# Kernel optimization log

Measured on AMD Instinct MI355X. Metric: run time of the kernel, lower is better.

The kernel has to match this reference:

```python
import jax, jax.numpy as jnp
import numpy as np

N = 50000          # nodes
E = 800000         # edges (avg degree 16)
F = 128            # in_dim = num_hidden*heads = pred_dim
H = 4              # attention heads per layer
D = 32             # num_hidden (per-head dim)
R = 11             # rel_num
L = 2              # num_layers
SCALE = float(1.0 / np.sqrt(D))


def setup_inputs() -> dict:
    key = jax.random.key(0)
    ks = jax.random.split(key, 16)
    inputs = jax.random.normal(ks[0], (N, F), jnp.float32)
    edge_types = jax.random.randint(ks[1], (E,), 0, R)
    src = jax.random.randint(ks[2], (E,), 0, N)
    dst = jax.random.randint(ks[3], (E,), 0, N)
    centrality = jax.random.uniform(ks[4], (N,), jnp.float32)
    rel_emb = jax.random.normal(ks[5], (R, F), jnp.float32) * 0.1
    # stacked per-layer projection weights (both layers have F -> H*D = F)
    Wq = jax.random.normal(ks[6], (L, F, H * D), jnp.float32) * 0.05
    Wk = jax.random.normal(ks[7], (L, F, H * D), jnp.float32) * 0.05
    Wv = jax.random.normal(ks[8], (L, F, H * D), jnp.float32) * 0.05
    We = jax.random.normal(ks[9], (L, F, H * D), jnp.float32) * 0.05
    bq = jnp.zeros((L, H * D), jnp.float32)
    bk = jnp.zeros((L, H * D), jnp.float32)
    bv = jnp.zeros((L, H * D), jnp.float32)
    be = jnp.zeros((L, H * D), jnp.float32)
    W_out = jax.random.normal(ks[10], (H * D, 1), jnp.float32) * 0.05
    b_out = jnp.zeros((1,), jnp.float32)
    gamma = jnp.ones((1,), jnp.float32)
    beta = jnp.zeros((1,), jnp.float32)
    return {"inputs": inputs, "edge_types": edge_types, "src": src, "dst": dst,
            "centrality": centrality, "rel_emb": rel_emb,
            "Wq": Wq, "bq": bq, "Wk": Wk, "bk": bk, "Wv": Wv, "bv": bv,
            "We": We, "be": be, "W_out": W_out, "b_out": b_out,
            "gamma": gamma, "beta": beta}


def _segment_softmax(score, dst, n):
    # score: [E, H]; softmax over incoming edges of each dst node
    m = jax.ops.segment_max(score, dst, num_segments=n)          # [N, H]
    ex = jnp.exp(score - m[dst])                                  # [E, H]
    s = jax.ops.segment_sum(ex, dst, num_segments=n)              # [N, H]
    return ex / (s[dst] + 1e-9)


def reference(inputs, edge_types, src, dst, centrality, rel_emb,
              Wq, bq, Wk, bk, Wv, bv, We, be, W_out, b_out, gamma, beta):
    h = inputs                                   # [N, F]
    ef = rel_emb[edge_types]                     # [E, pred_dim] relational edge embedding
    for l in range(L):
        q = (h @ Wq[l] + bq[l]).reshape(N, H, D)
        k = (h @ Wk[l] + bk[l]).reshape(N, H, D)
        v = (h @ Wv[l] + bv[l]).reshape(N, H, D)
        e = (ef @ We[l] + be[l]).reshape(E, H, D)
        # edge_mode="add": edge features added to keys/values on each edge
        ke = k[src] + e                           # [E, H, D]
        score = jnp.sum(q[dst] * ke, axis=-1) * SCALE   # [E, H]
        attn = _segment_softmax(score, dst, N)          # [E, H]
        msg = attn[:, :, None] * (v[src] + e)           # [E, H, D]
        agg = jax.ops.segment_sum(msg, dst, num_segments=N)  # [N, H, D]
        # identity residual (in_dim == H*D) + ELU activation
        h = jax.nn.elu(agg.reshape(N, H * D) + h)
    logits = h @ W_out + b_out                    # [N, 1]
    logits = jax.nn.relu((centrality * gamma + beta)[:, None] * logits)
    return logits
```

## Files before the change

### kernel.cpp

```cpp
#include <hip/hip_runtime.h>
#include <hip/hip_bf16.h>
#include <math.h>

#define SCALE_C 0.17677669529663687f
#define CAPP 64

typedef short bf16x8 __attribute__((ext_vector_type(8)));
typedef float f32x4 __attribute__((ext_vector_type(4)));


__global__ __launch_bounds__(256) void prep_scatter_k(
    const float* __restrict__ Wq, const float* __restrict__ Wk, const float* __restrict__ Wv,
    __hip_bfloat16* __restrict__ wf,
    const float* __restrict__ rel_emb, const float* __restrict__ We, const float* __restrict__ be,
    float* __restrict__ re, int R, int reb,
    const int* __restrict__ dst, const int* __restrict__ src, const int* __restrict__ etype,
    int E, int* __restrict__ cnt, int* __restrict__ bins) {
  int b = blockIdx.x;
  if (b < 48) {
    int tid = b * 256 + threadIdx.x;
    int lane = tid & 63;
    int frag = tid >> 6;
    int ks = frag & 3;
    int ct = (frag >> 2) & 7;
    int mat = frag >> 5;
    int l = mat / 3, m = mat % 3;
    const float* W = ((m == 0) ? Wq : (m == 1) ? Wk : Wv) + (size_t)l * 128 * 128;
    int nn = ct * 16 + (lane & 15);
    int k0 = ks * 32 + (lane >> 4) * 8;
    __hip_bfloat16 tmp[8];
    #pragma unroll
    for (int j = 0; j < 8; ++j) tmp[j] = __float2bfloat16(W[(size_t)(k0 + j) * 128 + nn]);
    *(uint4*)&wf[(size_t)frag * 64 * 8 + (size_t)lane * 8] = *(const uint4*)tmp;
  } else if (b < 48 + reb) {
    int idx = (b - 48) * 256 + threadIdx.x;
    int tot = 2 * R * 128;
    if (idx >= tot) return;
    int c = idx & 127;
    int r = (idx >> 7) % R;
    int l = idx / (R * 128);
    const float* W = We + (size_t)l * 128 * 128;
    float acc = be[l * 128 + c];
    #pragma unroll 4
    for (int kk = 0; kk < 128; ++kk) acc += rel_emb[r * 128 + kk] * W[kk * 128 + c];
    re[idx] = acc;
  } else {
    int e = (b - 48 - reb) * 256 + threadIdx.x;
    if (e < E) {
      int d = dst[e];
      int pos = atomicAdd(&cnt[d], 1);
      if (pos < CAPP) bins[(d << 6) + pos] = src[e] | (etype[e] << 20);
    }
  }
}


__device__ __forceinline__ void qkv_body(
    const float* __restrict__ Xf, const __hip_bfloat16* __restrict__ Xb,
    const __hip_bfloat16* __restrict__ wf,
    const float* __restrict__ bq, const float* __restrict__ bk, const float* __restrict__ bv,
    __hip_bfloat16* __restrict__ qo, __hip_bfloat16* __restrict__ kvo, int n, int bid) {
  __shared__ __hip_bfloat16 kvt[2][32][264];
  int wid = threadIdx.x >> 6;
  int lane = threadIdx.x & 63;
  int row0 = bid * 64 + wid * 32;
  if (row0 >= n) return;
  int cl = lane & 15;
  int quad = lane >> 4;

  bf16x8 afrag[2][4];
  #pragma unroll
  for (int s = 0; s < 2; ++s) {
    int arow = row0 + s * 16 + cl;
    bool av = arow < n;
    if (Xb) {
      const __hip_bfloat16* xr = Xb + (size_t)arow * 128 + quad * 8;
      #pragma unroll
      for (int ks = 0; ks < 4; ++ks) {
        uint4 raw = av ? *(const uint4*)(xr + ks * 32) : make_uint4(0, 0, 0, 0);
        afrag[s][ks] = __builtin_bit_cast(bf16x8, raw);
      }
    } else {
      const float* xr = Xf + (size_t)arow * 128 + quad * 8;
      #pragma unroll
      for (int ks = 0; ks < 4; ++ks) {
        float4 x0 = av ? *(const float4*)(xr + ks * 32)     : make_float4(0.f, 0.f, 0.f, 0.f);
        float4 x1 = av ? *(const float4*)(xr + ks * 32 + 4) : make_float4(0.f, 0.f, 0.f, 0.f);
        union { bf16x8 v; __hip_bfloat16 h[8]; } fu;
        fu.h[0] = __float2bfloat16(x0.x); fu.h[1] = __float2bfloat16(x0.y);
        fu.h[2] = __float2bfloat16(x0.z); fu.h[3] = __float2bfloat16(x0.w);
        fu.h[4] = __float2bfloat16(x1.x); fu.h[5] = __float2bfloat16(x1.y);
        fu.h[6] = __float2bfloat16(x1.z); fu.h[7] = __float2bfloat16(x1.w);
        afrag[s][ks] = fu.v;
      }
    }
  }
  const uint4* wfu = (const uint4*)wf;

  #pragma unroll
  for (int ct = 0; ct < 8; ++ct) {
    f32x4 a0 = {0.f, 0.f, 0.f, 0.f}, a1 = {0.f, 0.f, 0.f, 0.f};
    #pragma unroll
    for (int ks = 0; ks < 4; ++ks) {
      uint4 braw = wfu[((size_t)ct * 4 + ks) * 64 + lane];
      bf16x8 bfr = __builtin_bit_cast(bf16x8, braw);
      a0 = __builtin_amdgcn_mfma_f32_16x16x32_bf16(afrag[0][ks], bfr, a0, 0, 0, 0);
      a1 = __builtin_amdgcn_mfma_f32_16x16x32_bf16(afrag[1][ks], bfr, a1, 0, 0, 0);
    }
    int c = ct * 16 + cl;
    float bb = bq[c];
    #pragma unroll
    for (int r = 0; r < 4; ++r) {
      kvt[wid][quad * 4 + r][c]      = __float2bfloat16((a0[r] + bb) * SCALE_C);
      kvt[wid][16 + quad * 4 + r][c] = __float2bfloat16((a1[r] + bb) * SCALE_C);
    }
  }
  {
    const uint4* tsrc = (const uint4*)&kvt[wid][0][0];
    #pragma unroll
    for (int it = 0; it < 8; ++it) {
      int idx = it * 64 + lane;
      int row = idx >> 4, g = idx & 15;
      if (row0 + row < n)
        *(uint4*)&qo[((size_t)(row0 + row)) * 128 + g * 8] = tsrc[row * 33 + g];
    }
  }

  #pragma unroll
  for (int m = 1; m <= 2; ++m) {
    const float* bias = (m == 1) ? bk : bv;
    #pragma unroll
    for (int ct = 0; ct < 8; ++ct) {
      f32x4 a0 = {0.f, 0.f, 0.f, 0.f}, a1 = {0.f, 0.f, 0.f, 0.f};
      #pragma unroll
      for (int ks = 0; ks < 4; ++ks) {
        uint4 braw = wfu[((size_t)(m * 8 + ct) * 4 + ks) * 64 + lane];
        bf16x8 bfr = __builtin_bit_cast(bf16x8, braw);
        a0 = __builtin_amdgcn_mfma_f32_16x16x32_bf16(afrag[0][ks], bfr, a0, 0, 0, 0);
        a1 = __builtin_amdgcn_mfma_f32_16x16x32_bf16(afrag[1][ks], bfr, a1, 0, 0, 0);
      }
      int c = ct * 16 + cl;
      float bb = bias[c];
      int p = 8 * (c >> 2) + (c & 3) + ((m == 2) ? 4 : 0);
      #pragma unroll
      for (int r = 0; r < 4; ++r) {
        kvt[wid][quad * 4 + r][p]      = __float2bfloat16(a0[r] + bb);
        kvt[wid][16 + quad * 4 + r][p] = __float2bfloat16(a1[r] + bb);
      }
    }
  }
  {
    const uint4* tsrc = (const uint4*)&kvt[wid][0][0];
    #pragma unroll
    for (int it = 0; it < 16; ++it) {
      int idx = it * 64 + lane;
      int row = idx >> 5, off = idx & 31;
      if (row0 + row < n)
        *(uint4*)&kvo[((size_t)(row0 + row)) * 256 + off * 8] = tsrc[row * 33 + off];
    }
  }
}

__global__ __launch_bounds__(128) void qkv1_k(
    const float* __restrict__ Xf, const __hip_bfloat16* __restrict__ wf,
    const float* __restrict__ bq, const float* __restrict__ bk, const float* __restrict__ bv,
    __hip_bfloat16* __restrict__ qo, __hip_bfloat16* __restrict__ kvo, int n) {
  qkv_body(Xf, nullptr, wf, bq, bk, bv, qo, kvo, n, blockIdx.x);
}

__global__ __launch_bounds__(128) void qkv2_k(
    const __hip_bfloat16* __restrict__ Xb, const __hip_bfloat16* __restrict__ wf,
    const float* __restrict__ bq, const float* __restrict__ bk, const float* __restrict__ bv,
    __hip_bfloat16* __restrict__ qo, __hip_bfloat16* __restrict__ kvo, int n) {
  qkv_body(nullptr, Xb, wf, bq, bk, bv, qo, kvo, n, blockIdx.x);
}


__global__ __launch_bounds__(256) void edge_k(
    const __hip_bfloat16* __restrict__ qb, const __hip_bfloat16* __restrict__ kv,
    const float* __restrict__ re,
    const int* __restrict__ bins, const int* __restrict__ cnt,
    const float* __restrict__ h_in_f, const __hip_bfloat16* __restrict__ h_in_b,
    __hip_bfloat16* __restrict__ h_out_b,
    const float* __restrict__ Wout, const float* __restrict__ bout,
    const float* __restrict__ cent, const float* __restrict__ gamma,
    const float* __restrict__ beta, float* __restrict__ outp, int n) {
  int node = blockIdx.x * 4 + (threadIdx.x >> 6);
  if (node >= n) return;
  int lane = threadIdx.x & 63;
  int j = lane & 15;
  int quarter = lane >> 4;
  int rs = node << 6;
  int deg = cnt[node];
  deg = deg < CAPP ? deg : CAPP;

  uint4 qraw = *((const uint4*)(qb + ((size_t)node << 7)) + j);
  float qa0 = __uint_as_float(qraw.x << 16), qa1 = __uint_as_float(qraw.x & 0xffff0000u);
  float qa2 = __uint_as_float(qraw.y << 16), qa3 = __uint_as_float(qraw.y & 0xffff0000u);
  float qa4 = __uint_as_float(qraw.z << 16), qa5 = __uint_as_float(qraw.z & 0xffff0000u);
  float qa6 = __uint_as_float(qraw.w << 16), qa7 = __uint_as_float(qraw.w & 0xffff0000u);

  float ssum = 0.f;
  float acc0 = 0.f, acc1 = 0.f, acc2 = 0.f, acc3 = 0.f;
  float acc4 = 0.f, acc5 = 0.f, acc6 = 0.f, acc7 = 0.f;
  int nit = (deg + 3) >> 2;

  int pk1 = (quarter < deg) ? bins[rs + quarter] : 0;
  int pk2 = (quarter + 4 < deg) ? bins[rs + quarter + 4] : 0;
  uint s0 = (uint)pk1 & 0xFFFFFu, t0 = (uint)pk1 >> 20;
  const uint4* kr0 = (const uint4*)kv + (s0 * 32u + (uint)(j * 2));
  uint4 raw0 = kr0[0];
  uint4 raw1 = kr0[1];
  const float4* rr0 = (const float4*)re + (t0 * 32u + (uint)(j * 2));
  float4 r0 = rr0[0];
  float4 r1 = rr0[1];
  pk1 = pk2;

  for (int i = 0; i < nit; ++i) {
    int e2 = 4 * (i + 2) + quarter;
    pk2 = (e2 < deg) ? bins[rs + e2] : 0;
    uint s1 = (uint)pk1 & 0xFFFFFu, t1 = (uint)pk1 >> 20;
    const uint4* krn = (const uint4*)kv + (s1 * 32u + (uint)(j * 2));
    uint4 nraw0 = krn[0];
    uint4 nraw1 = krn[1];
    const float4* rrn = (const float4*)re + (t1 * 32u + (uint)(j * 2));
    float4 nr0 = rrn[0];
    float4 nr1 = rrn[1];

    bool valid = 4 * i + quarter < deg;
    float k0 = __uint_as_float(raw0.x << 16);
    float k1 = __uint_as_float(raw0.x & 0xffff0000u);
    float k2 = __uint_as_float(raw0.y << 16);
    float k3 = __uint_as_float(raw0.y & 0xffff0000u);
    float v0 = __uint_as_float(raw0.z << 16);
    float v1 = __uint_as_float(raw0.z & 0xffff0000u);
    float v2 = __uint_as_float(raw0.w << 16);
    float v3 = __uint_as_float(raw0.w & 0xffff0000u);
    float k4 = __uint_as_float(raw1.x << 16);
    float k5 = __uint_as_float(raw1.x & 0xffff0000u);
    float k6 = __uint_as_float(raw1.y << 16);
    float k7 = __uint_as_float(raw1.y & 0xffff0000u);
    float v4 = __uint_as_float(raw1.z << 16);
    float v5 = __uint_as_float(raw1.z & 0xffff0000u);
    float v6 = __uint_as_float(raw1.w << 16);
    float v7 = __uint_as_float(raw1.w & 0xffff0000u);
    float p = qa0 * (k0 + r0.x) + qa1 * (k1 + r0.y) + qa2 * (k2 + r0.z) + qa3 * (k3 + r0.w)
            + qa4 * (k4 + r1.x) + qa5 * (k5 + r1.y) + qa6 * (k6 + r1.z) + qa7 * (k7 + r1.w);
    p += __shfl_xor(p, 1);
    p += __shfl_xor(p, 2);
    float w = valid ? __expf(p) : 0.f;
    ssum += w;
    acc0 += w * (v0 + r0.x);
    acc1 += w * (v1 + r0.y);
    acc2 += w * (v2 + r0.z);
    acc3 += w * (v3 + r0.w);
    acc4 += w * (v4 + r1.x);
    acc5 += w * (v5 + r1.y);
    acc6 += w * (v6 + r1.z);
    acc7 += w * (v7 + r1.w);

    raw0 = nraw0; raw1 = nraw1; r0 = nr0; r1 = nr1;
    pk1 = pk2;
  }
  ssum += __shfl_xor(ssum, 16); ssum += __shfl_xor(ssum, 32);
  acc0 += __shfl_xor(acc0, 16); acc0 += __shfl_xor(acc0, 32);
  acc1 += __shfl_xor(acc1, 16); acc1 += __shfl_xor(acc1, 32);
  acc2 += __shfl_xor(acc2, 16); acc2 += __shfl_xor(acc2, 32);
  acc3 += __shfl_xor(acc3, 16); acc3 += __shfl_xor(acc3, 32);
  acc4 += __shfl_xor(acc4, 16); acc4 += __shfl_xor(acc4, 32);
  acc5 += __shfl_xor(acc5, 16); acc5 += __shfl_xor(acc5, 32);
  acc6 += __shfl_xor(acc6, 16); acc6 += __shfl_xor(acc6, 32);
  acc7 += __shfl_xor(acc7, 16); acc7 += __shfl_xor(acc7, 32);
  if (quarter != 0) return;

  float inv = 1.f / (ssum + 1e-9f);
  float4 h0, h1;
  if (h_in_b) {
    uint4 hraw = *((const uint4*)(h_in_b + ((size_t)node << 7)) + j);
    h0.x = __uint_as_float(hraw.x << 16); h0.y = __uint_as_float(hraw.x & 0xffff0000u);
    h0.z = __uint_as_float(hraw.y << 16); h0.w = __uint_as_float(hraw.y & 0xffff0000u);
    h1.x = __uint_as_float(hraw.z << 16); h1.y = __uint_as_float(hraw.z & 0xffff0000u);
    h1.z = __uint_as_float(hraw.w << 16); h1.w = __uint_as_float(hraw.w & 0xffff0000u);
  } else {
    const float4* hrow = (const float4*)h_in_f + ((uint)node * 32u + (uint)(j * 2));
    h0 = hrow[0]; h1 = hrow[1];
  }
  float x0 = acc0 * inv + h0.x;
  float x1 = acc1 * inv + h0.y;
  float x2 = acc2 * inv + h0.z;
  float x3 = acc3 * inv + h0.w;
  float x4 = acc4 * inv + h1.x;
  float x5 = acc5 * inv + h1.y;
  float x6 = acc6 * inv + h1.z;
  float x7 = acc7 * inv + h1.w;
  x0 = x0 > 0.f ? x0 : expm1f(x0);
  x1 = x1 > 0.f ? x1 : expm1f(x1);
  x2 = x2 > 0.f ? x2 : expm1f(x2);
  x3 = x3 > 0.f ? x3 : expm1f(x3);
  x4 = x4 > 0.f ? x4 : expm1f(x4);
  x5 = x5 > 0.f ? x5 : expm1f(x5);
  x6 = x6 > 0.f ? x6 : expm1f(x6);
  x7 = x7 > 0.f ? x7 : expm1f(x7);
  if (outp == nullptr) {
    union { uint4 u; __hip_bfloat16 hh[8]; } P;
    P.hh[0] = __float2bfloat16(x0); P.hh[1] = __float2bfloat16(x1);
    P.hh[2] = __float2bfloat16(x2); P.hh[3] = __float2bfloat16(x3);
    P.hh[4] = __float2bfloat16(x4); P.hh[5] = __float2bfloat16(x5);
    P.hh[6] = __float2bfloat16(x6); P.hh[7] = __float2bfloat16(x7);
    *((uint4*)(h_out_b + ((size_t)node << 7)) + j) = P.u;
  } else {
    const float4* wrow = (const float4*)Wout + (uint)(j * 2);
    float4 w0 = wrow[0], w1 = wrow[1];
    float pp = x0 * w0.x + x1 * w0.y + x2 * w0.z + x3 * w0.w
             + x4 * w1.x + x5 * w1.y + x6 * w1.z + x7 * w1.w;
    pp += __shfl_xor(pp, 1);
    pp += __shfl_xor(pp, 2);
    pp += __shfl_xor(pp, 4);
    pp += __shfl_xor(pp, 8);
    if (lane == 0) {
      float lg = pp + bout[0];
      lg *= (cent[node] * gamma[0] + beta[0]);
      outp[node] = fmaxf(lg, 0.f);
    }
  }
}


extern "C" void kernel_launch(void* const* d_in, const int* in_sizes, int n_in,
                              void* d_out, int out_size, void* d_ws, size_t ws_size,
                              hipStream_t stream) {
  const float* inputs  = (const float*)d_in[0];
  const int*   etype   = (const int*)d_in[1];
  const int*   src     = (const int*)d_in[2];
  const int*   dst     = (const int*)d_in[3];
  const float* cent    = (const float*)d_in[4];
  const float* rel_emb = (const float*)d_in[5];
  const float* Wq      = (const float*)d_in[6];
  const float* bq      = (const float*)d_in[7];
  const float* Wk      = (const float*)d_in[8];
  const float* bk      = (const float*)d_in[9];
  const float* Wv      = (const float*)d_in[10];
  const float* bv      = (const float*)d_in[11];
  const float* We      = (const float*)d_in[12];
  const float* be      = (const float*)d_in[13];
  const float* Wout    = (const float*)d_in[14];
  const float* bout    = (const float*)d_in[15];
  const float* gamma   = (const float*)d_in[16];
  const float* beta    = (const float*)d_in[17];
  float* out = (float*)d_out;

  const int N = in_sizes[0] / 128;
  const int E = in_sizes[1];
  const int R = in_sizes[5] / 128;

  float* re = (float*)d_ws;
  __hip_bfloat16* hb = (__hip_bfloat16*)(re + 2 * (size_t)R * 128);
  __hip_bfloat16* qb = hb + (size_t)N * 128;
  __hip_bfloat16* kv = qb + (size_t)N * 128;
  __hip_bfloat16* wf = kv + (size_t)N * 256;
  int* cnt  = (int*)(wf + 6 * 16384);
  int* bins = cnt + N;

  hipMemsetAsync(cnt, 0, (size_t)N * sizeof(int), stream);

  int reb = (2 * R * 128 + 255) / 256;
  int SB  = (E + 255) / 256;
  prep_scatter_k<<<48 + reb + SB, 256, 0, stream>>>(Wq, Wk, Wv, wf, rel_emb, We, be, re, R, reb,
                                                    dst, src, etype, E, cnt, bins);

  int QB = (N + 63) / 64;
  int eb = (N + 3) / 4;
  qkv1_k<<<QB, 128, 0, stream>>>(inputs, wf, bq, bk, bv, qb, kv, N);
  edge_k<<<eb, 256, 0, stream>>>(qb, kv, re, bins, cnt,
                                 inputs, nullptr, hb,
                                 Wout, bout, cent, gamma, beta, nullptr, N);
  qkv2_k<<<QB, 128, 0, stream>>>(hb, wf + (size_t)3 * 16384,
                                 bq + 128, bk + 128, bv + 128, qb, kv, N);
  edge_k<<<eb, 256, 0, stream>>>(qb, kv, re + (size_t)R * 128, bins, cnt,
                                 nullptr, hb, nullptr,
                                 Wout, bout, cent, gamma, beta, out, N);
}
```

Measured before the change: 309.0 us.

## Store q/kv/relation embeddings as fp16 and use packed half adds in edge loop

Switches the intermediate q, k, v buffers from bf16 to fp16 and the precomputed relation-edge embedding table from fp32 to fp16. In the edge aggregation loop the key+edge and value+edge sums become packed half-precision adds, which halves the relation-table load and cuts unpacking ALU work. Bin loads and source indices are now fetched unconditionally, with clamping in place of predication. This trades fp16 range/precision in the intermediates for fewer bytes loaded and fewer instructions, and it reads stale bin slots beyond the node's degree, which the later validity mask discards.

```diff
diff --git a/kernel.cpp b/kernel.cpp
--- a/kernel.cpp
+++ b/kernel.cpp
@@ -7,13 +7,16 @@
 
 typedef short bf16x8 __attribute__((ext_vector_type(8)));
 typedef float f32x4 __attribute__((ext_vector_type(4)));
+typedef _Float16 h16x2 __attribute__((ext_vector_type(2)));
+
+__device__ __forceinline__ h16x2 bch2(unsigned u) { return __builtin_bit_cast(h16x2, u); }
 
 
 __global__ __launch_bounds__(256) void prep_scatter_k(
     const float* __restrict__ Wq, const float* __restrict__ Wk, const float* __restrict__ Wv,
     __hip_bfloat16* __restrict__ wf,
     const float* __restrict__ rel_emb, const float* __restrict__ We, const float* __restrict__ be,
-    float* __restrict__ re, int R, int reb,
+    _Float16* __restrict__ re, int R, int reb,
     const int* __restrict__ dst, const int* __restrict__ src, const int* __restrict__ etype,
     int E, int* __restrict__ cnt, int* __restrict__ bins) {
   int b = blockIdx.x;
@@ -43,7 +46,7 @@
     float acc = be[l * 128 + c];
     #pragma unroll 4
     for (int kk = 0; kk < 128; ++kk) acc += rel_emb[r * 128 + kk] * W[kk * 128 + c];
-    re[idx] = acc;
+    re[idx] = (_Float16)acc;
   } else {
     int e = (b - 48 - reb) * 256 + threadIdx.x;
     if (e < E) {
@@ -59,8 +62,8 @@
     const float* __restrict__ Xf, const __hip_bfloat16* __restrict__ Xb,
     const __hip_bfloat16* __restrict__ wf,
     const float* __restrict__ bq, const float* __restrict__ bk, const float* __restrict__ bv,
-    __hip_bfloat16* __restrict__ qo, __hip_bfloat16* __restrict__ kvo, int n, int bid) {
-  __shared__ __hip_bfloat16 kvt[2][32][264];
+    _Float16* __restrict__ qo, _Float16* __restrict__ kvo, int n, int bid) {
+  __shared__ _Float16 kvt[2][32][264];
   int wid = threadIdx.x >> 6;
   int lane = threadIdx.x & 63;
   int row0 = bid * 64 + wid * 32;
@@ -111,8 +114,8 @@
     float bb = bq[c];
     #pragma unroll
     for (int r = 0; r < 4; ++r) {
-      kvt[wid][quad * 4 + r][c]      = __float2bfloat16((a0[r] + bb) * SCALE_C);
-      kvt[wid][16 + quad * 4 + r][c] = __float2bfloat16((a1[r] + bb) * SCALE_C);
+      kvt[wid][quad * 4 + r][c]      = (_Float16)((a0[r] + bb) * SCALE_C);
+      kvt[wid][16 + quad * 4 + r][c] = (_Float16)((a1[r] + bb) * SCALE_C);
     }
   }
   {
@@ -144,8 +147,8 @@
       int p = 8 * (c >> 2) + (c & 3) + ((m == 2) ? 4 : 0);
       #pragma unroll
       for (int r = 0; r < 4; ++r) {
-        kvt[wid][quad * 4 + r][p]      = __float2bfloat16(a0[r] + bb);
-        kvt[wid][16 + quad * 4 + r][p] = __float2bfloat16(a1[r] + bb);
+        kvt[wid][quad * 4 + r][p]      = (_Float16)(a0[r] + bb);
+        kvt[wid][16 + quad * 4 + r][p] = (_Float16)(a1[r] + bb);
       }
     }
   }
@@ -164,21 +167,21 @@
 __global__ __launch_bounds__(128) void qkv1_k(
     const float* __restrict__ Xf, const __hip_bfloat16* __restrict__ wf,
     const float* __restrict__ bq, const float* __restrict__ bk, const float* __restrict__ bv,
-    __hip_bfloat16* __restrict__ qo, __hip_bfloat16* __restrict__ kvo, int n) {
+    _Float16* __restrict__ qo, _Float16* __restrict__ kvo, int n) {
   qkv_body(Xf, nullptr, wf, bq, bk, bv, qo, kvo, n, blockIdx.x);
 }
 
 __global__ __launch_bounds__(128) void qkv2_k(
     const __hip_bfloat16* __restrict__ Xb, const __hip_bfloat16* __restrict__ wf,
     const float* __restrict__ bq, const float* __restrict__ bk, const float* __restrict__ bv,
-    __hip_bfloat16* __restrict__ qo, __hip_bfloat16* __restrict__ kvo, int n) {
+    _Float16* __restrict__ qo, _Float16* __restrict__ kvo, int n) {
   qkv_body(nullptr, Xb, wf, bq, bk, bv, qo, kvo, n, blockIdx.x);
 }
 
 
 __global__ __launch_bounds__(256) void edge_k(
-    const __hip_bfloat16* __restrict__ qb, const __hip_bfloat16* __restrict__ kv,
-    const float* __restrict__ re,
+    const _Float16* __restrict__ qb, const _Float16* __restrict__ kv,
+    const _Float16* __restrict__ re,
     const int* __restrict__ bins, const int* __restrict__ cnt,
     const float* __restrict__ h_in_f, const __hip_bfloat16* __restrict__ h_in_b,
     __hip_bfloat16* __restrict__ h_out_b,
@@ -193,73 +196,76 @@
   int rs = node << 6;
   int deg = cnt[node];
   deg = deg < CAPP ? deg : CAPP;
+  uint nm1 = (uint)(n - 1);
 
   uint4 qraw = *((const uint4*)(qb + ((size_t)node << 7)) + j);
-  float qa0 = __uint_as_float(qraw.x << 16), qa1 = __uint_as_float(qraw.x & 0xffff0000u);
-  float qa2 = __uint_as_float(qraw.y << 16), qa3 = __uint_as_float(qraw.y & 0xffff0000u);
-  float qa4 = __uint_as_float(qraw.z << 16), qa5 = __uint_as_float(qraw.z & 0xffff0000u);
-  float qa6 = __uint_as_float(qraw.w << 16), qa7 = __uint_as_float(qraw.w & 0xffff0000u);
+  h16x2 q01 = bch2(qraw.x), q23 = bch2(qraw.y), q45 = bch2(qraw.z), q67 = bch2(qraw.w);
+  float qa0 = (float)q01.x, qa1 = (float)q01.y;
+  float qa2 = (float)q23.x, qa3 = (float)q23.y;
+  float qa4 = (float)q45.x, qa5 = (float)q45.y;
+  float qa6 = (float)q67.x, qa7 = (float)q67.y;
 
   float ssum = 0.f;
   float acc0 = 0.f, acc1 = 0.f, acc2 = 0.f, acc3 = 0.f;
   float acc4 = 0.f, acc5 = 0.f, acc6 = 0.f, acc7 = 0.f;
   int nit = (deg + 3) >> 2;
 
-  int pk1 = (quarter < deg) ? bins[rs + quarter] : 0;
-  int pk2 = (quarter + 4 < deg) ? bins[rs + quarter + 4] : 0;
-  uint s0 = (uint)pk1 & 0xFFFFFu, t0 = (uint)pk1 >> 20;
-  const uint4* kr0 = (const uint4*)kv + (s0 * 32u + (uint)(j * 2));
-  uint4 raw0 = kr0[0];
-  uint4 raw1 = kr0[1];
-  const float4* rr0 = (const float4*)re + (t0 * 32u + (uint)(j * 2));
-  float4 r0 = rr0[0];
-  float4 r1 = rr0[1];
+  const uint4* kvb = (const uint4*)kv + (uint)(j * 2);
+  const uint4* reb = (const uint4*)re + (uint)j;
+
+  int pk1 = bins[rs + quarter];
+  int pk2 = bins[rs + quarter + 4];
+  uint s0 = (uint)pk1 & 0xFFFFFu; s0 = s0 < nm1 ? s0 : nm1;
+  uint t0 = (uint)pk1 >> 20;
+  uint4 raw0 = kvb[s0 * 32u];
+  uint4 raw1 = kvb[s0 * 32u + 1u];
+  uint4 rr   = reb[t0 * 16u];
   pk1 = pk2;
 
   for (int i = 0; i < nit; ++i) {
-    int e2 = 4 * (i + 2) + quarter;
-    pk2 = (e2 < deg) ? bins[rs + e2] : 0;
-    uint s1 = (uint)pk1 & 0xFFFFFu, t1 = (uint)pk1 >> 20;
-    const uint4* krn = (const uint4*)kv + (s1 * 32u + (uint)(j * 2));
-    uint4 nraw0 = krn[0];
-    uint4 nraw1 = krn[1];
-    const float4* rrn = (const float4*)re + (t1 * 32u + (uint)(j * 2));
-    float4 nr0 = rrn[0];
-    float4 nr1 = rrn[1];
-
-    bool valid = 4 * i + quarter < deg;
-    float k0 = __uint_as_float(raw0.x << 16);
-    float k1 = __uint_as_float(raw0.x & 0xffff0000u);
-    float k2 = __uint_as_float(raw0.y << 16);
-    float k3 = __uint_as_float(raw0.y & 0xffff0000u);
-    float v0 = __uint_as_float(raw0.z << 16);
-    float v1 = __uint_as_float(raw0.z & 0xffff0000u);
-    float v2 = __uint_as_float(raw0.w << 16);
-    float v3 = __uint_as_float(raw0.w & 0xffff0000u);
-    float k4 = __uint_as_float(raw1.x << 16);
-    float k5 = __uint_as_float(raw1.x & 0xffff0000u);
-    float k6 = __uint_as_float(raw1.y << 16);
-    float k7 = __uint_as_float(raw1.y & 0xffff0000u);
-    float v4 = __uint_as_float(raw1.z << 16);
-    float v5 = __uint_as_float(raw1.z & 0xffff0000u);
-    float v6 = __uint_as_float(raw1.w << 16);
-    float v7 = __uint_as_float(raw1.w & 0xffff0000u);
-    float p = qa0 * (k0 + r0.x) + qa1 * (k1 + r0.y) + qa2 * (k2 + r0.z) + qa3 * (k3 + r0.w)
-            + qa4 * (k4 + r1.x) + qa5 * (k5 + r1.y) + qa6 * (k6 + r1.z) + qa7 * (k7 + r1.w);
+    int e2 = 4 * i + 8 + quarter;
+    e2 = e2 < 63 ? e2 : 63;
+    pk2 = bins[rs + e2];
+    uint s1 = (uint)pk1 & 0xFFFFFu; s1 = s1 < nm1 ? s1 : nm1;
+    uint t1 = (uint)pk1 >> 20;
+    uint4 nraw0 = kvb[s1 * 32u];
+    uint4 nraw1 = kvb[s1 * 32u + 1u];
+    uint4 nrr   = reb[t1 * 16u];
+
+    h16x2 r01 = bch2(rr.x), r23 = bch2(rr.y), r45 = bch2(rr.z), r67 = bch2(rr.w);
+    h16x2 kr01 = bch2(raw0.x) + r01;
+    h16x2 kr23 = bch2(raw0.y) + r23;
+    h16x2 kr45 = bch2(raw1.x) + r45;
+    h16x2 kr67 = bch2(raw1.y) + r67;
+    h16x2 vr01 = bch2(raw0.z) + r01;
+    h16x2 vr23 = bch2(raw0.w) + r23;
+    h16x2 vr45 = bch2(raw1.z) + r45;
+    h16x2 vr67 = bch2(raw1.w) + r67;
+
+    float pA = qa0 * (float)kr01.x;
+    pA += qa1 * (float)kr01.y;
+    pA += qa2 * (float)kr23.x;
+    pA += qa3 * (float)kr23.y;
+    float pB = qa4 * (float)kr45.x;
+    pB += qa5 * (float)kr45.y;
+    pB += qa6 * (float)kr67.x;
+    pB += qa7 * (float)kr67.y;
+    float p = pA + pB;
     p += __shfl_xor(p, 1);
     p += __shfl_xor(p, 2);
+    bool valid = 4 * i + quarter < deg;
     float w = valid ? __expf(p) : 0.f;
     ssum += w;
-    acc0 += w * (v0 + r0.x);
-    acc1 += w * (v1 + r0.y);
-    acc2 += w * (v2 + r0.z);
-    acc3 += w * (v3 + r0.w);
-    acc4 += w * (v4 + r1.x);
-    acc5 += w * (v5 + r1.y);
-    acc6 += w * (v6 + r1.z);
-    acc7 += w * (v7 + r1.w);
-
-    raw0 = nraw0; raw1 = nraw1; r0 = nr0; r1 = nr1;
+    acc0 += w * (float)vr01.x;
+    acc1 += w * (float)vr01.y;
+    acc2 += w * (float)vr23.x;
+    acc3 += w * (float)vr23.y;
+    acc4 += w * (float)vr45.x;
+    acc5 += w * (float)vr45.y;
+    acc6 += w * (float)vr67.x;
+    acc7 += w * (float)vr67.y;
+
+    raw0 = nraw0; raw1 = nraw1; rr = nrr;
     pk1 = pk2;
   }
   ssum += __shfl_xor(ssum, 16); ssum += __shfl_xor(ssum, 32);
@@ -353,11 +359,11 @@
   const int E = in_sizes[1];
   const int R = in_sizes[5] / 128;
 
-  float* re = (float*)d_ws;
+  _Float16* re = (_Float16*)d_ws;
   __hip_bfloat16* hb = (__hip_bfloat16*)(re + 2 * (size_t)R * 128);
-  __hip_bfloat16* qb = hb + (size_t)N * 128;
-  __hip_bfloat16* kv = qb + (size_t)N * 128;
-  __hip_bfloat16* wf = kv + (size_t)N * 256;
+  _Float16* qb = (_Float16*)(hb + (size_t)N * 128);
+  _Float16* kv = qb + (size_t)N * 128;
+  __hip_bfloat16* wf = (__hip_bfloat16*)(kv + (size_t)N * 256);
   int* cnt  = (int*)(wf + 6 * 16384);
   int* bins = cnt + N;
 
```

Result: faster. 302.8 us (-2.0%).
